# Kernel tuning notes

Hardware: AMD Instinct MI355X
Metric: run time of the kernel (lower is better)

Reference implementation:

```python
import jax, jax.numpy as jnp
import numpy as np

B, F, MP, P = 4, 9, 100, 12000   # batch, point feats, max_points, max_pillars
C = 64                            # nb_channels
NY = NX = 400                     # canvas
EPS = 1e-3
POOL_W = 100                      # encoder MaxPool2d kernel (1, max_points)


def setup_inputs() -> dict:
    key = jax.random.key(0)
    ks = jax.random.split(key, 12)
    x = jax.random.normal(ks[0], (B, F, MP, P), dtype=jnp.float32)
    # coords[:, 0]=batch id, [:,2]=y, [:,3]=x ; unique (y,x) per batch so scatter is well-defined
    rng = np.random.default_rng(0)
    coords = np.zeros((B * P, 4), dtype=np.int32)
    for b in range(B):
        lin = rng.choice(NY * NX, size=P, replace=False)
        coords[b * P:(b + 1) * P, 0] = b
        coords[b * P:(b + 1) * P, 2] = lin // NX
        coords[b * P:(b + 1) * P, 3] = lin % NX
    coords = jnp.asarray(coords)
    w1 = jax.random.normal(ks[1], (C, F), dtype=jnp.float32) * 0.1
    b1 = jax.random.normal(ks[2], (C,), dtype=jnp.float32) * 0.1
    g1 = 1.0 + 0.1 * jax.random.normal(ks[3], (C,), dtype=jnp.float32)
    be1 = 0.1 * jax.random.normal(ks[4], (C,), dtype=jnp.float32)
    m1 = 0.1 * jax.random.normal(ks[5], (C,), dtype=jnp.float32)
    v1 = 0.5 + jax.random.uniform(ks[6], (C,), dtype=jnp.float32)
    w2 = jax.random.normal(ks[7], (C, C), dtype=jnp.float32) * 0.1
    b2 = jax.random.normal(ks[8], (C,), dtype=jnp.float32) * 0.1
    g2 = 1.0 + 0.1 * jax.random.normal(ks[9], (C,), dtype=jnp.float32)
    be2 = 0.1 * jax.random.normal(ks[10], (C,), dtype=jnp.float32)
    m2 = 0.1 * jax.random.normal(ks[11], (C,), dtype=jnp.float32)
    v2 = 0.5 + jax.random.uniform(jax.random.fold_in(key, 99), (C,), dtype=jnp.float32)
    return {"x": x, "coords": coords, "w1": w1, "b1": b1, "g1": g1, "be1": be1,
            "m1": m1, "v1": v1, "w2": w2, "b2": b2, "g2": g2, "be2": be2,
            "m2": m2, "v2": v2}


def _bn_scale_shift(g, be, m, v):
    s = g * jax.lax.rsqrt(v + EPS)
    return s, be - m * s


def reference(x, coords, w1, b1, g1, be1, m1, v1, w2, b2, g2, be2, m2, v2):
    # ---- MiniPointNet: conv1x1 + BN(eval) + ReLU + maxpool over points ----
    s1, t1 = _bn_scale_shift(g1, be1, m1, v1)
    h = jnp.einsum('bfhw,cf->bchw', x, w1) + b1[None, :, None, None]
    h = jax.nn.relu(h * s1[None, :, None, None] + t1[None, :, None, None])
    feat = jnp.max(h, axis=2)                       # [B, C, P]
    # ---- PointPillarsScatter (vectorized over batch) ----
    voxels = feat.transpose(0, 2, 1).reshape(B * P, C)   # [B*P, C]
    flat = (coords[:, 0].astype(jnp.int32) * (NY * NX)
            + coords[:, 2].astype(jnp.int32) * NX
            + coords[:, 3].astype(jnp.int32))
    canvas = jnp.zeros((B * NY * NX, C), dtype=voxels.dtype).at[flat].set(voxels)
    canvas = canvas.reshape(B, NY, NX, C).transpose(0, 3, 1, 2)  # [B, C, NY, NX]
    # ---- BackBoneEncoder: conv1x1 + BN(eval) + ReLU + maxpool (1, POOL_W) ----
    s2, t2 = _bn_scale_shift(g2, be2, m2, v2)
    h2 = jnp.einsum('bchw,dc->bdhw', canvas, w2) + b2[None, :, None, None]
    h2 = jax.nn.relu(h2 * s2[None, :, None, None] + t2[None, :, None, None])
    out = jnp.max(h2.reshape(B, C, NY, NX // POOL_W, POOL_W), axis=-1)  # [B,C,NY,NX/100]
    return out
```

## Files before the change

kernel.cpp:

```cpp
#include <hip/hip_runtime.h>
#include <hip/hip_bf16.h>

#define BB   4
#define FF   9
#define MPP  100
#define PP   12000
#define CC   64
#define NYY  400
#define NXO  4
#define NPIL (BB * PP)
#define NWIN (BB * NYY * NXO)

#define WS_CNT    0
#define WS_BIAS1  (NWIN * 4)
#define WS_BIAS2  (WS_BIAS1 + 256)
#define WS_W1PB   (WS_BIAS2 + 256)
#define WS_W2PB   (WS_W1PB + 2048)
#define WS_BINS   (WS_W2PB + 8192)
#define WS_FEAT2  (WS_BINS + 1280000)

typedef __attribute__((ext_vector_type(8)))  short short8;
typedef __attribute__((ext_vector_type(16))) float float16;

__device__ __forceinline__ short f2bf(float v) {
    __hip_bfloat16 h = __float2bfloat16(v);
    short s; __builtin_memcpy(&s, &h, 2); return s;
}
__device__ __forceinline__ float bf2f(unsigned short u) {
    return __int_as_float(((int)u) << 16);
}
__device__ __forceinline__ int fkey(float v) {
    int b = __float_as_int(v);
    return b >= 0 ? b : (b ^ 0x7fffffff);
}
__device__ __forceinline__ float kinv(int k) {
    return __int_as_float(k >= 0 ? k : (k ^ 0x7fffffff));
}

__global__ void prep_kernel(const float* __restrict__ w1, const float* __restrict__ b1,
                            const float* __restrict__ g1, const float* __restrict__ be1,
                            const float* __restrict__ m1, const float* __restrict__ v1,
                            const float* __restrict__ w2, const float* __restrict__ b2,
                            const float* __restrict__ g2, const float* __restrict__ be2,
                            const float* __restrict__ m2, const float* __restrict__ v2,
                            char* __restrict__ ws)
{
    float* bias1 = (float*)(ws + WS_BIAS1);
    float* bias2 = (float*)(ws + WS_BIAS2);
    short* w1pb  = (short*)(ws + WS_W1PB);
    short* w2pb  = (short*)(ws + WS_W2PB);
    const int t = threadIdx.x;
    if (t < 64) {
        const float s1 = g1[t] * rsqrtf(v1[t] + 1e-3f);
        bias1[t] = s1 * b1[t] + (be1[t] - m1[t] * s1);
        #pragma unroll
        for (int s = 0; s < 16; ++s) {
            const int f = (s < 4) ? s : ((s >= 8 && s < 13) ? s - 4 : -1);
            w1pb[t * 16 + s] = (f >= 0) ? f2bf(s1 * w1[t * 9 + f]) : (short)0;
        }
        const float s2 = g2[t] * rsqrtf(v2[t] + 1e-3f);
        bias2[t] = s2 * b2[t] + (be2[t] - m2[t] * s2);
    }
    for (int i = t; i < CC * CC; i += 256) {
        const int d = i >> 6;
        const float s2 = g2[d] * rsqrtf(v2[d] + 1e-3f);
        w2pb[i] = f2bf(s2 * w2[i]);
    }
}

#define LOAD5(dst, ptr) do { \
    dst##0 = __builtin_nontemporal_load((ptr)); \
    dst##1 = __builtin_nontemporal_load((ptr) + FS); \
    dst##2 = __builtin_nontemporal_load((ptr) + 2 * FS); \
    dst##3 = __builtin_nontemporal_load((ptr) + 3 * FS); \
    dst##4 = __builtin_nontemporal_load((ptr) + 4 * FS); } while (0)

#define BUILD_BF(bf, s_) do { \
    bf[0] = f2bf(s_##0); bf[1] = f2bf(s_##1); bf[2] = f2bf(s_##2); \
    bf[3] = f2bf(s_##3); bf[4] = half ? f2bf(s_##4) : (short)0; } while (0)

#define STEP2(sA, sB) do { \
    short8 bfA = (short8)0, bfB = (short8)0; \
    BUILD_BF(bfA, sA); BUILD_BF(bfB, sB); \
    const float16 z0A = __builtin_amdgcn_mfma_f32_32x32x16_bf16(af0, bfA, (float16)0.f, 0, 0, 0); \
    const float16 z1A = __builtin_amdgcn_mfma_f32_32x32x16_bf16(af1, bfA, (float16)0.f, 0, 0, 0); \
    const float16 z0B = __builtin_amdgcn_mfma_f32_32x32x16_bf16(af0, bfB, (float16)0.f, 0, 0, 0); \
    const float16 z1B = __builtin_amdgcn_mfma_f32_32x32x16_bf16(af1, bfB, (float16)0.f, 0, 0, 0); \
    _Pragma("unroll") \
    for (int r = 0; r < 16; ++r) { \
        vmx0[r] = fmaxf(fmaxf(vmx0[r], z0A[r]), z0B[r]); \
        vmx1[r] = fmaxf(fmaxf(vmx1[r], z1A[r]), z1B[r]); \
    } } while (0)

__global__ __launch_bounds__(256, 4) void pillar_kernel(
    const float* __restrict__ x, const int* __restrict__ coords,
    char* __restrict__ ws, int* __restrict__ cnt)
{
    __shared__ char  arena[8448];
    __shared__ short featbT[32 * 72];

    int*   red = (int*)arena;
    float* s2f = (float*)arena;

    const float* bias1 = (const float*)(ws + WS_BIAS1);
    const float* bias2 = (const float*)(ws + WS_BIAS2);
    const short* w1pb  = (const short*)(ws + WS_W1PB);
    const short* w2pb  = (const short*)(ws + WS_W2PB);
    unsigned short* bins  = (unsigned short*)(ws + WS_BINS);
    short*          feat2 = (short*)(ws + WS_FEAT2);

    const int t    = threadIdx.x;
    const int lane = t & 63;
    const int wv   = t >> 6;
    const int half = lane >> 5;
    const int pcol = lane & 31;
    const int v0   = blockIdx.x * 32;
    const int b    = v0 / PP;
    const int p0   = v0 - b * PP;

    #pragma unroll
    for (int i = 0; i < 8; ++i) red[i * 256 + t] = (int)0x80000000;

    if (t < 32) {
        const int* c4 = coords + (size_t)(v0 + t) * 4;
        const int w = (c4[0] * NYY + c4[2]) * NXO + c4[3] / 100;
        const int slot = atomicAdd(&cnt[w], 1);
        bins[w * 100 + slot] = (unsigned short)(v0 + t);
    }
    __syncthreads();

    const short8 af0 = *(const short8*)(w1pb + pcol * 16 + half * 8);
    const short8 af1 = *(const short8*)(w1pb + (pcol + 32) * 16 + half * 8);

    float16 vmx0, vmx1;
    #pragma unroll
    for (int r = 0; r < 16; ++r) { vmx0[r] = -3.0e38f; vmx1[r] = -3.0e38f; }

    const size_t FS = (size_t)MPP * PP;
    const float* q = x + (size_t)b * FF * FS
                       + (size_t)(wv * 25) * PP
                       + (size_t)half * 4 * FS
                       + p0 + pcol;

    float a_0, a_1, a_2, a_3, a_4, b_0, b_1, b_2, b_3, b_4;
    float c_0, c_1, c_2, c_3, c_4, d_0, d_1, d_2, d_3, d_4;
    LOAD5(a_, q); LOAD5(b_, q + PP); q += 2 * PP;
    LOAD5(c_, q); LOAD5(d_, q + PP); q += 2 * PP;

    for (int it = 0; it < 10; ++it) {
        float n0_0, n0_1, n0_2, n0_3, n0_4, n1_0, n1_1, n1_2, n1_3, n1_4;
        LOAD5(n0_, q); LOAD5(n1_, q + PP); q += 2 * PP;
        STEP2(a_, b_);
        a_0 = c_0; a_1 = c_1; a_2 = c_2; a_3 = c_3; a_4 = c_4;
        b_0 = d_0; b_1 = d_1; b_2 = d_2; b_3 = d_3; b_4 = d_4;
        c_0 = n0_0; c_1 = n0_1; c_2 = n0_2; c_3 = n0_3; c_4 = n0_4;
        d_0 = n1_0; d_1 = n1_1; d_2 = n1_2; d_3 = n1_3; d_4 = n1_4;
    }
    STEP2(a_, b_);
    STEP2(c_, d_);
    {
        LOAD5(a_, q);
        short8 bfA = (short8)0;
        BUILD_BF(bfA, a_);
        const float16 z0 = __builtin_amdgcn_mfma_f32_32x32x16_bf16(af0, bfA, (float16)0.f, 0, 0, 0);
        const float16 z1 = __builtin_amdgcn_mfma_f32_32x32x16_bf16(af1, bfA, (float16)0.f, 0, 0, 0);
        #pragma unroll
        for (int r = 0; r < 16; ++r) {
            vmx0[r] = fmaxf(vmx0[r], z0[r]);
            vmx1[r] = fmaxf(vmx1[r], z1[r]);
        }
    }

    #pragma unroll
    for (int r = 0; r < 16; ++r) {
        const int chl = (r & 3) + 8 * (r >> 2) + 4 * half;
        atomicMax(&red[chl * 32 + pcol],        fkey(vmx0[r]));
        atomicMax(&red[(chl + 32) * 32 + pcol], fkey(vmx1[r]));
    }
    __syncthreads();

    {
        const int p  = t & 31;
        const int cg = t >> 5;
        #pragma unroll
        for (int j = 0; j < 8; ++j) {
            const int c = cg * 8 + j;
            const float m = kinv(red[c * 32 + p]);
            featbT[p * 72 + c] = f2bf(fmaxf(0.f, m + bias1[c]));
        }
    }
    __syncthreads();

    if (wv < 2) {
        const short* wrow = w2pb + (wv * 32 + pcol) * 64 + half * 8;
        const short8 wa0 = *(const short8*)(wrow +  0);
        const short8 wa1 = *(const short8*)(wrow + 16);
        const short8 wa2 = *(const short8*)(wrow + 32);
        const short8 wa3 = *(const short8*)(wrow + 48);
        const short* frow = &featbT[pcol * 72 + half * 8];
        const short8 fb0 = *(const short8*)(frow +  0);
        const short8 fb1 = *(const short8*)(frow + 16);
        const short8 fb2 = *(const short8*)(frow + 32);
        const short8 fb3 = *(const short8*)(frow + 48);

        float16 acc = (float16)0.f;
        acc = __builtin_amdgcn_mfma_f32_32x32x16_bf16(wa0, fb0, acc, 0, 0, 0);
        acc = __builtin_amdgcn_mfma_f32_32x32x16_bf16(wa1, fb1, acc, 0, 0, 0);
        acc = __builtin_amdgcn_mfma_f32_32x32x16_bf16(wa2, fb2, acc, 0, 0, 0);
        acc = __builtin_amdgcn_mfma_f32_32x32x16_bf16(wa3, fb3, acc, 0, 0, 0);

        #pragma unroll
        for (int r = 0; r < 16; ++r) {
            const int d = wv * 32 + (r & 3) + 8 * (r >> 2) + 4 * half;
            s2f[pcol * 66 + d] = fmaxf(0.f, acc[r] + bias2[d]);
        }
    }
    __syncthreads();

    {
        const int p  = t >> 3;
        const int d0 = (t & 7) * 8;
        short8 o;
        #pragma unroll
        for (int j = 0; j < 8; ++j) o[j] = f2bf(s2f[p * 66 + d0 + j]);
        *(short8*)(feat2 + (size_t)(v0 + p) * 64 + d0) = o;
    }
}

__global__ __launch_bounds__(256) void gather_kernel(
    const char* __restrict__ ws, const int* __restrict__ cnt,
    float* __restrict__ out)
{
    const float* bias2 = (const float*)(ws + WS_BIAS2);
    const unsigned short* bins  = (const unsigned short*)(ws + WS_BINS);
    const unsigned short* feat2 = (const unsigned short*)(ws + WS_FEAT2);

    const int t  = threadIdx.x;
    const int wl = t & 63;
    const int dg = t >> 6;
    const int w  = blockIdx.x * 64 + wl;
    const int k  = cnt[w];

    float m[16];
    #pragma unroll
    for (int j = 0; j < 16; ++j) {
        const float zv = fmaxf(0.f, bias2[dg * 16 + j]);
        m[j] = (k >= 100) ? 0.f : zv;
    }
    int i = 0;
    for (; i + 2 <= k; i += 2) {
        const int pidA = bins[w * 100 + i];
        const int pidB = bins[w * 100 + i + 1];
        const unsigned short* rowA = feat2 + (size_t)pidA * 64 + dg * 16;
        const unsigned short* rowB = feat2 + (size_t)pidB * 64 + dg * 16;
        const short8 a0 = *(const short8*)(rowA);
        const short8 a1 = *(const short8*)(rowA + 8);
        const short8 b0 = *(const short8*)(rowB);
        const short8 b1 = *(const short8*)(rowB + 8);
        #pragma unroll
        for (int j = 0; j < 8; ++j) {
            m[j]     = fmaxf(fmaxf(m[j],     bf2f((unsigned short)a0[j])), bf2f((unsigned short)b0[j]));
            m[j + 8] = fmaxf(fmaxf(m[j + 8], bf2f((unsigned short)a1[j])), bf2f((unsigned short)b1[j]));
        }
    }
    if (i < k) {
        const int pid = bins[w * 100 + i];
        const unsigned short* row = feat2 + (size_t)pid * 64 + dg * 16;
        const short8 a0 = *(const short8*)(row);
        const short8 a1 = *(const short8*)(row + 8);
        #pragma unroll
        for (int j = 0; j < 8; ++j) {
            m[j]     = fmaxf(m[j],     bf2f((unsigned short)a0[j]));
            m[j + 8] = fmaxf(m[j + 8], bf2f((unsigned short)a1[j]));
        }
    }

    const int b   = w / (NYY * NXO);
    const int rem = w - b * (NYY * NXO);
    const int y   = rem >> 2;
    const int xo  = rem & 3;
    #pragma unroll
    for (int j = 0; j < 16; ++j) {
        const int d = dg * 16 + j;
        out[(((size_t)b * CC + d) * NYY + y) * NXO + xo] = m[j];
    }
}

extern "C" void kernel_launch(void* const* d_in, const int* in_sizes, int n_in,
                              void* d_out, int out_size, void* d_ws, size_t ws_size,
                              hipStream_t stream) {
    const float* x   = (const float*)d_in[0];
    const int*   cds = (const int*)d_in[1];
    const float* w1  = (const float*)d_in[2];
    const float* b1  = (const float*)d_in[3];
    const float* g1  = (const float*)d_in[4];
    const float* be1 = (const float*)d_in[5];
    const float* m1  = (const float*)d_in[6];
    const float* v1  = (const float*)d_in[7];
    const float* w2  = (const float*)d_in[8];
    const float* b2  = (const float*)d_in[9];
    const float* g2  = (const float*)d_in[10];
    const float* be2 = (const float*)d_in[11];
    const float* m2  = (const float*)d_in[12];
    const float* v2  = (const float*)d_in[13];

    char* ws = (char*)d_ws;
    int*  cnt = (int*)(ws + WS_CNT);

    hipMemsetAsync(cnt, 0, (size_t)NWIN * 4, stream);

    prep_kernel<<<1, 256, 0, stream>>>(w1, b1, g1, be1, m1, v1,
                                       w2, b2, g2, be2, m2, v2, ws);

    pillar_kernel<<<NPIL / 32, 256, 0, stream>>>(x, cds, ws, cnt);

    gather_kernel<<<NWIN / 64, 256, 0, stream>>>(ws, cnt, (float*)d_out);
}
```

Before: 277.5 us.

## Fold weight prep into pillar kernel with LDS-staged weights and vectorized bin reads

Drops the separate single-block prep kernel. Each pillar block now computes the BN-folded bf16 weights and biases itself and keeps them in shared memory, with a padded w2 row stride to reduce bank conflicts. The gather kernel recomputes bias2 from the raw BN parameters and reads bin indices four at a time. The fifth feature load of the lower half now reads a valid slice instead of one past it, so no separate prep launch is needed. The cost is redundant weight-folding work in every one of the 1500 pillar blocks, plus extra shared memory that may lower occupancy.

```diff
diff --git a/kernel.cpp b/kernel.cpp
--- a/kernel.cpp
+++ b/kernel.cpp
@@ -12,15 +12,12 @@
 #define NWIN (BB * NYY * NXO)
 
 #define WS_CNT    0
-#define WS_BIAS1  (NWIN * 4)
-#define WS_BIAS2  (WS_BIAS1 + 256)
-#define WS_W1PB   (WS_BIAS2 + 256)
-#define WS_W2PB   (WS_W1PB + 2048)
-#define WS_BINS   (WS_W2PB + 8192)
+#define WS_BINS   36352
 #define WS_FEAT2  (WS_BINS + 1280000)
 
 typedef __attribute__((ext_vector_type(8)))  short short8;
 typedef __attribute__((ext_vector_type(16))) float float16;
+typedef __attribute__((ext_vector_type(4)))  unsigned short ushort4v;
 
 __device__ __forceinline__ short f2bf(float v) {
     __hip_bfloat16 h = __float2bfloat16(v);
@@ -35,37 +32,6 @@
 }
 __device__ __forceinline__ float kinv(int k) {
     return __int_as_float(k >= 0 ? k : (k ^ 0x7fffffff));
-}
-
-__global__ void prep_kernel(const float* __restrict__ w1, const float* __restrict__ b1,
-                            const float* __restrict__ g1, const float* __restrict__ be1,
-                            const float* __restrict__ m1, const float* __restrict__ v1,
-                            const float* __restrict__ w2, const float* __restrict__ b2,
-                            const float* __restrict__ g2, const float* __restrict__ be2,
-                            const float* __restrict__ m2, const float* __restrict__ v2,
-                            char* __restrict__ ws)
-{
-    float* bias1 = (float*)(ws + WS_BIAS1);
-    float* bias2 = (float*)(ws + WS_BIAS2);
-    short* w1pb  = (short*)(ws + WS_W1PB);
-    short* w2pb  = (short*)(ws + WS_W2PB);
-    const int t = threadIdx.x;
-    if (t < 64) {
-        const float s1 = g1[t] * rsqrtf(v1[t] + 1e-3f);
-        bias1[t] = s1 * b1[t] + (be1[t] - m1[t] * s1);
-        #pragma unroll
-        for (int s = 0; s < 16; ++s) {
-            const int f = (s < 4) ? s : ((s >= 8 && s < 13) ? s - 4 : -1);
-            w1pb[t * 16 + s] = (f >= 0) ? f2bf(s1 * w1[t * 9 + f]) : (short)0;
-        }
-        const float s2 = g2[t] * rsqrtf(v2[t] + 1e-3f);
-        bias2[t] = s2 * b2[t] + (be2[t] - m2[t] * s2);
-    }
-    for (int i = t; i < CC * CC; i += 256) {
-        const int d = i >> 6;
-        const float s2 = g2[d] * rsqrtf(v2[d] + 1e-3f);
-        w2pb[i] = f2bf(s2 * w2[i]);
-    }
 }
 
 #define LOAD5(dst, ptr) do { \
@@ -73,7 +39,7 @@
     dst##1 = __builtin_nontemporal_load((ptr) + FS); \
     dst##2 = __builtin_nontemporal_load((ptr) + 2 * FS); \
     dst##3 = __builtin_nontemporal_load((ptr) + 3 * FS); \
-    dst##4 = __builtin_nontemporal_load((ptr) + 4 * FS); } while (0)
+    dst##4 = __builtin_nontemporal_load((ptr) + off4); } while (0)
 
 #define BUILD_BF(bf, s_) do { \
     bf[0] = f2bf(s_##0); bf[1] = f2bf(s_##1); bf[2] = f2bf(s_##2); \
@@ -94,18 +60,24 @@
 
 __global__ __launch_bounds__(256, 4) void pillar_kernel(
     const float* __restrict__ x, const int* __restrict__ coords,
+    const float* __restrict__ w1, const float* __restrict__ b1,
+    const float* __restrict__ g1, const float* __restrict__ be1,
+    const float* __restrict__ m1, const float* __restrict__ v1,
+    const float* __restrict__ w2, const float* __restrict__ b2,
+    const float* __restrict__ g2, const float* __restrict__ be2,
+    const float* __restrict__ m2, const float* __restrict__ v2,
     char* __restrict__ ws, int* __restrict__ cnt)
 {
     __shared__ char  arena[8448];
     __shared__ short featbT[32 * 72];
+    __shared__ short w1pb_s[64 * 16];
+    __shared__ short w2pb_s[64 * 80];
+    __shared__ float bias1_s[64];
+    __shared__ float bias2_s[64];
 
     int*   red = (int*)arena;
     float* s2f = (float*)arena;
 
-    const float* bias1 = (const float*)(ws + WS_BIAS1);
-    const float* bias2 = (const float*)(ws + WS_BIAS2);
-    const short* w1pb  = (const short*)(ws + WS_W1PB);
-    const short* w2pb  = (const short*)(ws + WS_W2PB);
     unsigned short* bins  = (unsigned short*)(ws + WS_BINS);
     short*          feat2 = (short*)(ws + WS_FEAT2);
 
@@ -127,16 +99,36 @@
         const int slot = atomicAdd(&cnt[w], 1);
         bins[w * 100 + slot] = (unsigned short)(v0 + t);
     }
+
+    if (t < 64) {
+        const float s1 = g1[t] * rsqrtf(v1[t] + 1e-3f);
+        bias1_s[t] = s1 * b1[t] + (be1[t] - m1[t] * s1);
+        #pragma unroll
+        for (int s = 0; s < 16; ++s) {
+            const int f = (s < 4) ? s : ((s >= 8 && s < 13) ? s - 4 : -1);
+            w1pb_s[t * 16 + s] = (f >= 0) ? f2bf(s1 * w1[t * 9 + f]) : (short)0;
+        }
+        const float s2 = g2[t] * rsqrtf(v2[t] + 1e-3f);
+        bias2_s[t] = s2 * b2[t] + (be2[t] - m2[t] * s2);
+    }
+    #pragma unroll
+    for (int i0 = 0; i0 < 16; ++i0) {
+        const int i = i0 * 256 + t;
+        const int d = i >> 6;
+        const float s2d = g2[d] * rsqrtf(v2[d] + 1e-3f);
+        w2pb_s[d * 80 + (i & 63)] = f2bf(s2d * w2[i]);
+    }
     __syncthreads();
 
-    const short8 af0 = *(const short8*)(w1pb + pcol * 16 + half * 8);
-    const short8 af1 = *(const short8*)(w1pb + (pcol + 32) * 16 + half * 8);
+    const short8 af0 = *(const short8*)(w1pb_s + pcol * 16 + half * 8);
+    const short8 af1 = *(const short8*)(w1pb_s + (pcol + 32) * 16 + half * 8);
 
     float16 vmx0, vmx1;
     #pragma unroll
     for (int r = 0; r < 16; ++r) { vmx0[r] = -3.0e38f; vmx1[r] = -3.0e38f; }
 
     const size_t FS = (size_t)MPP * PP;
+    const size_t off4 = (size_t)(half ? 4 : 3) * FS;
     const float* q = x + (size_t)b * FF * FS
                        + (size_t)(wv * 25) * PP
                        + (size_t)half * 4 * FS
@@ -186,13 +178,13 @@
         for (int j = 0; j < 8; ++j) {
             const int c = cg * 8 + j;
             const float m = kinv(red[c * 32 + p]);
-            featbT[p * 72 + c] = f2bf(fmaxf(0.f, m + bias1[c]));
+            featbT[p * 72 + c] = f2bf(fmaxf(0.f, m + bias1_s[c]));
         }
     }
     __syncthreads();
 
     if (wv < 2) {
-        const short* wrow = w2pb + (wv * 32 + pcol) * 64 + half * 8;
+        const short* wrow = &w2pb_s[(wv * 32 + pcol) * 80 + half * 8];
         const short8 wa0 = *(const short8*)(wrow +  0);
         const short8 wa1 = *(const short8*)(wrow + 16);
         const short8 wa2 = *(const short8*)(wrow + 32);
@@ -212,7 +204,7 @@
         #pragma unroll
         for (int r = 0; r < 16; ++r) {
             const int d = wv * 32 + (r & 3) + 8 * (r >> 2) + 4 * half;
-            s2f[pcol * 66 + d] = fmaxf(0.f, acc[r] + bias2[d]);
+            s2f[pcol * 66 + d] = fmaxf(0.f, acc[r] + bias2_s[d]);
         }
     }
     __syncthreads();
@@ -228,10 +220,12 @@
 }
 
 __global__ __launch_bounds__(256) void gather_kernel(
+    const float* __restrict__ g2, const float* __restrict__ b2,
+    const float* __restrict__ be2, const float* __restrict__ m2,
+    const float* __restrict__ v2,
     const char* __restrict__ ws, const int* __restrict__ cnt,
     float* __restrict__ out)
 {
-    const float* bias2 = (const float*)(ws + WS_BIAS2);
     const unsigned short* bins  = (const unsigned short*)(ws + WS_BINS);
     const unsigned short* feat2 = (const unsigned short*)(ws + WS_FEAT2);
 
@@ -244,34 +238,28 @@
     float m[16];
     #pragma unroll
     for (int j = 0; j < 16; ++j) {
-        const float zv = fmaxf(0.f, bias2[dg * 16 + j]);
+        const int d = dg * 16 + j;
+        const float s2 = g2[d] * rsqrtf(v2[d] + 1e-3f);
+        const float bias2d = s2 * b2[d] + (be2[d] - m2[d] * s2);
+        const float zv = fmaxf(0.f, bias2d);
         m[j] = (k >= 100) ? 0.f : zv;
     }
-    int i = 0;
-    for (; i + 2 <= k; i += 2) {
-        const int pidA = bins[w * 100 + i];
-        const int pidB = bins[w * 100 + i + 1];
-        const unsigned short* rowA = feat2 + (size_t)pidA * 64 + dg * 16;
-        const unsigned short* rowB = feat2 + (size_t)pidB * 64 + dg * 16;
-        const short8 a0 = *(const short8*)(rowA);
-        const short8 a1 = *(const short8*)(rowA + 8);
-        const short8 b0 = *(const short8*)(rowB);
-        const short8 b1 = *(const short8*)(rowB + 8);
-        #pragma unroll
-        for (int j = 0; j < 8; ++j) {
-            m[j]     = fmaxf(fmaxf(m[j],     bf2f((unsigned short)a0[j])), bf2f((unsigned short)b0[j]));
-            m[j + 8] = fmaxf(fmaxf(m[j + 8], bf2f((unsigned short)a1[j])), bf2f((unsigned short)b1[j]));
-        }
-    }
-    if (i < k) {
-        const int pid = bins[w * 100 + i];
-        const unsigned short* row = feat2 + (size_t)pid * 64 + dg * 16;
-        const short8 a0 = *(const short8*)(row);
-        const short8 a1 = *(const short8*)(row + 8);
-        #pragma unroll
-        for (int j = 0; j < 8; ++j) {
-            m[j]     = fmaxf(m[j],     bf2f((unsigned short)a0[j]));
-            m[j + 8] = fmaxf(m[j + 8], bf2f((unsigned short)a1[j]));
+
+    const unsigned short* brow = bins + (size_t)w * 100;
+    for (int i = 0; i < k; i += 4) {
+        const ushort4v p4 = *(const ushort4v*)(brow + i);
+        #pragma unroll
+        for (int j = 0; j < 4; ++j) {
+            if (i + j < k) {
+                const unsigned short* row = feat2 + (size_t)p4[j] * 64 + dg * 16;
+                const short8 a0 = *(const short8*)(row);
+                const short8 a1 = *(const short8*)(row + 8);
+                #pragma unroll
+                for (int jj = 0; jj < 8; ++jj) {
+                    m[jj]     = fmaxf(m[jj],     bf2f((unsigned short)a0[jj]));
+                    m[jj + 8] = fmaxf(m[jj + 8], bf2f((unsigned short)a1[jj]));
+                }
+            }
         }
     }
 
@@ -309,10 +297,11 @@
 
     hipMemsetAsync(cnt, 0, (size_t)NWIN * 4, stream);
 
-    prep_kernel<<<1, 256, 0, stream>>>(w1, b1, g1, be1, m1, v1,
-                                       w2, b2, g2, be2, m2, v2, ws);
-
-    pillar_kernel<<<NPIL / 32, 256, 0, stream>>>(x, cds, ws, cnt);
-
-    gather_kernel<<<NWIN / 64, 256, 0, stream>>>(ws, cnt, (float*)d_out);
-}
+    pillar_kernel<<<NPIL / 32, 256, 0, stream>>>(x, cds,
+                                                 w1, b1, g1, be1, m1, v1,
+                                                 w2, b2, g2, be2, m2, v2,
+                                                 ws, cnt);
+
+    gather_kernel<<<NWIN / 64, 256, 0, stream>>>(g2, b2, be2, m2, v2,
+                                                 ws, cnt, (float*)d_out);
+}
```

Result: no change. 274.7 us (-1.0%).
